# Kernel tuning notes

Measured on AMD Instinct MI355X. Metric: run time of the kernel, lower is better.

Reference implementation:

```python
import jax, jax.numpy as jnp
import numpy as np

EMB = 128
N_LEFT = 100000
N_RIGHT = 100000
N_EDGES = 600000
EDGE_FEAT = 1


def _ortho(key, shape):
    a = jax.random.normal(key, shape, dtype=jnp.float32)
    q, r = jnp.linalg.qr(a if shape[0] >= shape[1] else a.T)
    q = q * jnp.sign(jnp.diag(r))
    return q if shape[0] >= shape[1] else q.T


def setup_inputs() -> dict:
    key = jax.random.key(0)
    ks = jax.random.split(key, 12)
    return {
        "left_features": jax.random.normal(ks[0], (N_LEFT, EMB), dtype=jnp.float32),
        "edge_indices": jax.random.randint(ks[1], (2, N_EDGES), 0, N_LEFT, dtype=jnp.int32).astype(jnp.int64),
        "edge_features": jax.random.normal(ks[2], (N_EDGES, EDGE_FEAT), dtype=jnp.float32),
        "right_features": jax.random.normal(ks[3], (N_RIGHT, EMB), dtype=jnp.float32),
        "scatter_out_size": N_RIGHT,
        # parameters (orthogonal weights, zero biases, unit PreNorm scales)
        "W_left": _ortho(ks[4], (EMB, EMB)),
        "b_left": jnp.zeros((EMB,), jnp.float32),
        "W_edge": _ortho(ks[5], (EMB, EDGE_FEAT)),
        "W_right": _ortho(ks[6], (EMB, EMB)),
        "scale_final": jnp.ones((1,), jnp.float32),
        "W_final": _ortho(ks[7], (EMB, EMB)),
        "b_final": jnp.zeros((EMB,), jnp.float32),
        "scale_post": jnp.ones((1,), jnp.float32),
        "W_out1": _ortho(ks[8], (EMB, 2 * EMB)),
        "b_out1": jnp.zeros((EMB,), jnp.float32),
        "W_out2": _ortho(ks[9], (EMB, EMB)),
        "b_out2": jnp.zeros((EMB,), jnp.float32),
    }


def reference(left_features, edge_indices, edge_features, right_features,
              scatter_out_size, W_left, b_left, W_edge, W_right,
              scale_final, W_final, b_final, scale_post,
              W_out1, b_out1, W_out2, b_out2):
    # node / edge projections
    left_proj = left_features @ W_left.T + b_left            # [n_left, emb]
    edge_proj = edge_features @ W_edge.T                     # [n_edges, emb]
    right_proj = right_features @ W_right.T                  # [n_right, emb]
    # gather per-edge messages and combine
    joint = left_proj[edge_indices[0]] + edge_proj + right_proj[edge_indices[1]]
    # feature_module_final: PreNorm(scale only) -> ReLU -> Linear
    joint = jax.nn.relu(joint * scale_final) @ W_final.T + b_final
    # scatter-add onto right-side nodes (right_to_left=False)
    conv = jax.ops.segment_sum(joint, edge_indices[1], num_segments=scatter_out_size)
    conv = conv * scale_post
    # output MLP on [conv ; prev_right]
    h = jnp.concatenate([conv, right_features], axis=1)      # [n_right, 2*emb]
    h = jax.nn.relu(h @ W_out1.T + b_out1)
    return h @ W_out2.T + b_out2
```

## Files before the change

### kernel.cpp

```cpp
#include <hip/hip_runtime.h>

#define EMB 128

typedef __attribute__((ext_vector_type(8))) short short8;
typedef __attribute__((ext_vector_type(4))) short short4v;
typedef __attribute__((ext_vector_type(4))) float floatx4;

#define MFMA(a, b, c) __builtin_amdgcn_mfma_f32_16x16x32_bf16((a), (b), (c), 0, 0, 0)

__device__ __forceinline__ ushort f2b(float f) {
    unsigned u = __float_as_uint(f);
    return (ushort)((u + 0x7fff + ((u >> 16) & 1)) >> 16);
}
__device__ __forceinline__ float b2f(ushort h) {
    return __uint_as_float(((unsigned)h) << 16);
}
__device__ __forceinline__ short8 cvt8(const float* p) {
    float4 f0 = *(const float4*)p;
    float4 f1 = *(const float4*)(p + 4);
    short8 v;
    v[0] = f2b(f0.x); v[1] = f2b(f0.y); v[2] = f2b(f0.z); v[3] = f2b(f0.w);
    v[4] = f2b(f1.x); v[5] = f2b(f1.y); v[6] = f2b(f1.z); v[7] = f2b(f1.w);
    return v;
}

template <int RSH>
__device__ __forceinline__ void stage32k(const ushort* __restrict__ g,
                                         ushort* __restrict__ lds, int t) {
#pragma unroll
    for (int i = 0; i < 8; i++) {
        int a = i * 4096 + t * 16;
        short8 v = *(const short8*)(g + (a >> 1));
        int d = a ^ (((a >> RSH) & 7) << 4);
        *(short8*)((char*)lds + d) = v;
    }
}
__device__ __forceinline__ short8 ldsW8(const ushort* lds, int byte) {
    return *(const short8*)((const char*)lds + (byte ^ (((byte >> 8) & 7) << 4)));
}
__device__ __forceinline__ short8 ldsW9(const ushort* lds, int byte) {
    return *(const short8*)((const char*)lds + (byte ^ (((byte >> 9) & 7) << 4)));
}

__global__ __launch_bounds__(256) void k_cvthist(const float* __restrict__ w0,
                                                 const float* __restrict__ w1,
                                                 const float* __restrict__ w2,
                                                 const float* __restrict__ w3,
                                                 const float* __restrict__ w4,
                                                 ushort* __restrict__ dst,
                                                 const int* __restrict__ eidx,
                                                 int* __restrict__ cnt,
                                                 int n_edges) {
    int bid = blockIdx.x;
    if (bid < 384) {
        int i = bid * 256 + threadIdx.x;
        const float* src; int off;
        if (i < 16384)      { src = w0; off = i; }
        else if (i < 32768) { src = w1; off = i - 16384; }
        else if (i < 49152) { src = w2; off = i - 32768; }
        else if (i < 81920) { src = w3; off = i - 49152; }
        else                { src = w4; off = i - 81920; }
        dst[i] = f2b(src[off]);
    } else {
        int e = (bid - 384) * 256 + threadIdx.x;
        if (e < n_edges) atomicAdd(&cnt[eidx[n_edges + e]], 1);
    }
}

#define SCAN_CHUNK 4096
__global__ __launch_bounds__(1024) void k_scan1(const int* __restrict__ cnt,
                                                int* __restrict__ offs,
                                                int* __restrict__ bsum, int n) {
    __shared__ int buf[1024];
    int t = threadIdx.x;
    int i0 = blockIdx.x * SCAN_CHUNK + t * 4;
    int v[4];
#pragma unroll
    for (int u = 0; u < 4; u++) { int i = i0 + u; v[u] = (i < n) ? cnt[i] : 0; }
    int s = v[0] + v[1] + v[2] + v[3];
    buf[t] = s;
    __syncthreads();
    for (int d = 1; d < 1024; d <<= 1) {
        int x = (t >= d) ? buf[t - d] : 0;
        __syncthreads();
        buf[t] += x;
        __syncthreads();
    }
    int excl = buf[t] - s;
#pragma unroll
    for (int u = 0; u < 4; u++) { int i = i0 + u; if (i < n) offs[i] = excl; excl += v[u]; }
    if (t == 1023) bsum[blockIdx.x] = buf[1023];
}

__global__ __launch_bounds__(1024) void k_scan2(const int* __restrict__ bsum,
                                                int* __restrict__ offs,
                                                int* __restrict__ cursor, int n) {
    int bid = blockIdx.x;
    int base = 0;
    for (int j = 0; j < bid; j++) base += bsum[j];
    int i0 = bid * SCAN_CHUNK + threadIdx.x * 4;
#pragma unroll
    for (int u = 0; u < 4; u++) {
        int i = i0 + u;
        if (i < n) { int o = offs[i] + base; offs[i] = o; cursor[i] = o; }
    }
}

__global__ __launch_bounds__(256) void k_permproj(const int* __restrict__ eidx,
                                                  const float* __restrict__ ef,
                                                  int* __restrict__ cursor,
                                                  int2* __restrict__ sle,
                                                  int n_edges,
                                                  const float* __restrict__ XL,
                                                  const float* __restrict__ XR,
                                                  const ushort* __restrict__ WLb,
                                                  const ushort* __restrict__ WRb,
                                                  const float* __restrict__ bias,
                                                  ushort* __restrict__ YL,
                                                  ushort* __restrict__ YR,
                                                  int n, int eb, int nblk) {
    __shared__ ushort Wlds[16384];
    int bid = blockIdx.x;
    if (bid < eb) {
        int e = bid * 256 + threadIdx.x;
        if (e < n_edges) {
            int r = eidx[n_edges + e];
            int p = atomicAdd(&cursor[r], 1);
            int2 v; v.x = eidx[e]; v.y = __float_as_int(ef[e]);
            sle[p] = v;
        }
        return;
    }
    bid -= eb;
    const float* X; const ushort* Wb; ushort* Y; int has_bias;
    if (bid < nblk) { X = XL; Wb = WLb; Y = YL; has_bias = 1; }
    else            { X = XR; Wb = WRb; Y = YR; has_bias = 0; bid -= nblk; }

    int t = threadIdx.x, wave = t >> 6, lane = t & 63;
    int m = lane & 15, quad = lane >> 4;
    size_t row0 = (size_t)bid * 64;
    size_t row = row0 + wave * 16 + m;
    size_t rowc = (row < (size_t)n) ? row : (size_t)(n - 1);

    stage32k<8>(Wb, Wlds, t);

    short8 xf[4];
    const float* xr = X + rowc * EMB;
#pragma unroll
    for (int ks = 0; ks < 4; ks++)
        xf[ks] = cvt8(xr + ks * 32 + quad * 8);

    __syncthreads();

    bool ok = (row < (size_t)n);
#pragma unroll
    for (int wt = 0; wt < 8; wt++) {
        floatx4 acc = {0.f, 0.f, 0.f, 0.f};
#pragma unroll
        for (int ks = 0; ks < 4; ks++) {
            short8 w = ldsW8(Wlds, ((wt * 16 + m) << 8) + (ks << 6) + (quad << 4));
            acc = MFMA(w, xf[ks], acc);
        }
        float b0 = 0.f, b1_ = 0.f, b2_ = 0.f, b3 = 0.f;
        if (has_bias) {
            float4 bb = *(const float4*)(bias + wt * 16 + quad * 4);
            b0 = bb.x; b1_ = bb.y; b2_ = bb.z; b3 = bb.w;
        }
        if (ok) {
            short4v o;
            o[0] = f2b(acc[0] + b0);
            o[1] = f2b(acc[1] + b1_);
            o[2] = f2b(acc[2] + b2_);
            o[3] = f2b(acc[3] + b3);
            *(short4v*)(Y + row * EMB + wt * 16 + quad * 4) = o;
        }
    }
}

__global__ __launch_bounds__(256) void k_reduce(const ushort* __restrict__ Pl,
                                                const ushort* __restrict__ Pr,
                                                const int2* __restrict__ sle,
                                                const float* __restrict__ We,
                                                const int* __restrict__ offs,
                                                const float* __restrict__ scale_final,
                                                ushort* __restrict__ S,
                                                int n_right, int n_edges) {
    int r = blockIdx.x * 4 + (threadIdx.x >> 6);
    if (r >= n_right) return;
    int lane = threadIdx.x & 63;
    int g = lane >> 4;
    int m = lane & 15;
    float scale = scale_final[0];

    float4 w0 = *(const float4*)(We + m * 8);
    float4 w1 = *(const float4*)(We + m * 8 + 4);
    short8 prv = *(const short8*)(Pr + (size_t)r * EMB + m * 8);
    float we[8], pr[8];
    we[0] = w0.x; we[1] = w0.y; we[2] = w0.z; we[3] = w0.w;
    we[4] = w1.x; we[5] = w1.y; we[6] = w1.z; we[7] = w1.w;
#pragma unroll
    for (int j = 0; j < 8; j++) pr[j] = b2f((ushort)prv[j]);

    float acc[8] = {0.f, 0.f, 0.f, 0.f, 0.f, 0.f, 0.f, 0.f};
    int s0 = offs[r];
    int s1 = (r + 1 < n_right) ? offs[r + 1] : n_edges;
    int e = s0 + g;
    for (; e + 4 < s1; e += 8) {
        int2 ea = sle[e];
        int2 eb = sle[e + 4];
        short8 pa = *(const short8*)(Pl + (size_t)ea.x * EMB + m * 8);
        short8 pb = *(const short8*)(Pl + (size_t)eb.x * EMB + m * 8);
        float fa = __int_as_float(ea.y), fb = __int_as_float(eb.y);
#pragma unroll
        for (int j = 0; j < 8; j++) {
            acc[j] += fmaxf((b2f((ushort)pa[j]) + pr[j] + fa * we[j]) * scale, 0.f);
            acc[j] += fmaxf((b2f((ushort)pb[j]) + pr[j] + fb * we[j]) * scale, 0.f);
        }
    }
    if (e < s1) {
        int2 ea = sle[e];
        short8 pa = *(const short8*)(Pl + (size_t)ea.x * EMB + m * 8);
        float fa = __int_as_float(ea.y);
#pragma unroll
        for (int j = 0; j < 8; j++)
            acc[j] += fmaxf((b2f((ushort)pa[j]) + pr[j] + fa * we[j]) * scale, 0.f);
    }
#pragma unroll
    for (int j = 0; j < 8; j++) {
        acc[j] += __shfl_xor(acc[j], 16);
        acc[j] += __shfl_xor(acc[j], 32);
    }
    if (g == 0) {
        short8 o;
#pragma unroll
        for (int j = 0; j < 8; j++) o[j] = f2b(acc[j]);
        *(short8*)(S + (size_t)r * EMB + m * 8) = o;
    }
}

__global__ __launch_bounds__(256) void k_out(const ushort* __restrict__ S,
                                             const float* __restrict__ right,
                                             const ushort* __restrict__ Wfb,
                                             const float* __restrict__ bf,
                                             const int* __restrict__ deg,
                                             const float* __restrict__ sc_post,
                                             const ushort* __restrict__ W1b,
                                             const float* __restrict__ b1,
                                             const ushort* __restrict__ W2b,
                                             const float* __restrict__ b2,
                                             float* __restrict__ out, int n) {
    __shared__ ushort Wlds[16384];
    __shared__ ushort H[64][136];
    __shared__ float degs[64];
    int t = threadIdx.x, wave = t >> 6, lane = t & 63;
    int m = lane & 15, quad = lane >> 4;
    size_t row0 = (size_t)blockIdx.x * 64;
    int rl = wave * 16 + m;
    size_t xrow = row0 + rl;
    size_t xrowc = (xrow < (size_t)n) ? xrow : (size_t)(n - 1);
    bool ok = (xrow < (size_t)n);
    float sp = sc_post[0];

    short8 s4[4], ar[4];
    const ushort* sr = S + xrowc * EMB;
    const float* rr = right + xrowc * EMB;
#pragma unroll
    for (int ks = 0; ks < 4; ks++)
        s4[ks] = *(const short8*)(sr + ks * 32 + quad * 8);
    stage32k<8>(Wfb, Wlds, t);
#pragma unroll
    for (int ks = 0; ks < 4; ks++)
        ar[ks] = cvt8(rr + ks * 32 + quad * 8);
    if (t < 64) {
        size_t rr2 = row0 + t;
        degs[t] = (rr2 < (size_t)n) ? (float)deg[rr2] : 0.f;
    }
    __syncthreads();
    float dd = degs[rl];

#pragma unroll
    for (int wt = 0; wt < 8; wt++) {
        floatx4 acc = {0.f, 0.f, 0.f, 0.f};
#pragma unroll
        for (int ks = 0; ks < 4; ks++) {
            short8 w = ldsW8(Wlds, ((wt * 16 + m) << 8) + (ks << 6) + (quad << 4));
            acc = MFMA(w, s4[ks], acc);
        }
        float4 bb = *(const float4*)(bf + wt * 16 + quad * 4);
        short4v o;
        o[0] = f2b((acc[0] + dd * bb.x) * sp);
        o[1] = f2b((acc[1] + dd * bb.y) * sp);
        o[2] = f2b((acc[2] + dd * bb.z) * sp);
        o[3] = f2b((acc[3] + dd * bb.w) * sp);
        *(short4v*)(&H[rl][wt * 16 + quad * 4]) = o;
    }
    short8 c4[4];
#pragma unroll
    for (int ks = 0; ks < 4; ks++)
        c4[ks] = *(const short8*)(&H[rl][ks * 32 + quad * 8]);
    __syncthreads();
    stage32k<9>(W1b, Wlds, t);
    __syncthreads();

#pragma unroll
    for (int wt = 0; wt < 4; wt++) {
        floatx4 acc = {0.f, 0.f, 0.f, 0.f};
        int rb = wt * 16 + m;
#pragma unroll
        for (int ks = 0; ks < 4; ks++) {
            short8 w = ldsW9(Wlds, (rb << 9) + (ks << 6) + (quad << 4));
            acc = MFMA(w, c4[ks], acc);
        }
#pragma unroll
        for (int ks = 0; ks < 4; ks++) {
            short8 w = ldsW9(Wlds, (rb << 9) + 256 + (ks << 6) + (quad << 4));
            acc = MFMA(w, ar[ks], acc);
        }
        float4 bb = *(const float4*)(b1 + wt * 16 + quad * 4);
        short4v o;
        o[0] = f2b(fmaxf(acc[0] + bb.x, 0.f));
        o[1] = f2b(fmaxf(acc[1] + bb.y, 0.f));
        o[2] = f2b(fmaxf(acc[2] + bb.z, 0.f));
        o[3] = f2b(fmaxf(acc[3] + bb.w, 0.f));
        *(short4v*)(&H[rl][wt * 16 + quad * 4]) = o;
    }
    __syncthreads();
    stage32k<9>(W1b + 16384, Wlds, t);
    __syncthreads();

#pragma unroll
    for (int wt = 4; wt < 8; wt++) {
        floatx4 acc = {0.f, 0.f, 0.f, 0.f};
        int rb = (wt - 4) * 16 + m;
#pragma unroll
        for (int ks = 0; ks < 4; ks++) {
            short8 w = ldsW9(Wlds, (rb << 9) + (ks << 6) + (quad << 4));
            acc = MFMA(w, c4[ks], acc);
        }
#pragma unroll
        for (int ks = 0; ks < 4; ks++) {
            short8 w = ldsW9(Wlds, (rb << 9) + 256 + (ks << 6) + (quad << 4));
            acc = MFMA(w, ar[ks], acc);
        }
        float4 bb = *(const float4*)(b1 + wt * 16 + quad * 4);
        short4v o;
        o[0] = f2b(fmaxf(acc[0] + bb.x, 0.f));
        o[1] = f2b(fmaxf(acc[1] + bb.y, 0.f));
        o[2] = f2b(fmaxf(acc[2] + bb.z, 0.f));
        o[3] = f2b(fmaxf(acc[3] + bb.w, 0.f));
        *(short4v*)(&H[rl][wt * 16 + quad * 4]) = o;
    }
    short8 h4[4];
#pragma unroll
    for (int ks = 0; ks < 4; ks++)
        h4[ks] = *(const short8*)(&H[rl][ks * 32 + quad * 8]);
    __syncthreads();
    stage32k<8>(W2b, Wlds, t);
    __syncthreads();

#pragma unroll
    for (int wt = 0; wt < 8; wt++) {
        floatx4 acc = {0.f, 0.f, 0.f, 0.f};
#pragma unroll
        for (int ks = 0; ks < 4; ks++) {
            short8 w = ldsW8(Wlds, ((wt * 16 + m) << 8) + (ks << 6) + (quad << 4));
            acc = MFMA(w, h4[ks], acc);
        }
        if (ok) {
            float4 bb = *(const float4*)(b2 + wt * 16 + quad * 4);
            float4 o;
            o.x = acc[0] + bb.x;
            o.y = acc[1] + bb.y;
            o.z = acc[2] + bb.z;
            o.w = acc[3] + bb.w;
            *(float4*)(out + xrow * EMB + wt * 16 + quad * 4) = o;
        }
    }
}

extern "C" void kernel_launch(void* const* d_in, const int* in_sizes, int n_in,
                              void* d_out, int out_size, void* d_ws, size_t ws_size,
                              hipStream_t stream) {
    const float* left   = (const float*)d_in[0];
    const int*   eidx   = (const int*)  d_in[1];
    const float* efeat  = (const float*)d_in[2];
    const float* right  = (const float*)d_in[3];
    const float* W_left = (const float*)d_in[5];
    const float* b_left = (const float*)d_in[6];
    const float* W_edge = (const float*)d_in[7];
    const float* W_right= (const float*)d_in[8];
    const float* sc_fin = (const float*)d_in[9];
    const float* W_fin  = (const float*)d_in[10];
    const float* b_fin  = (const float*)d_in[11];
    const float* sc_post= (const float*)d_in[12];
    const float* W_out1 = (const float*)d_in[13];
    const float* b_out1 = (const float*)d_in[14];
    const float* W_out2 = (const float*)d_in[15];
    const float* b_out2 = (const float*)d_in[16];

    int n_left  = in_sizes[0] / EMB;
    int n_edges = in_sizes[2];
    int n_right = in_sizes[3] / EMB;

    ushort* us = (ushort*)d_ws;
    ushort* Wl_b = us;
    ushort* Wr_b = us + 16384;
    ushort* Wf_b = us + 32768;
    ushort* W1_b = us + 49152;
    ushort* W2_b = us + 81920;
    ushort* Pl   = us + 98304;
    ushort* Pr   = Pl + (size_t)n_left * EMB;
    ushort* S    = Pr + (size_t)n_right * EMB;
    int* cnt    = (int*)(S + (size_t)n_right * EMB);
    int* offs   = cnt + n_right;
    int* cursor = offs + n_right;
    int* bsum   = cursor + n_right;
    int2* sle   = (int2*)(bsum + 64);

    hipMemsetAsync(cnt, 0, (size_t)n_right * sizeof(int), stream);

    int eb = (n_edges + 255) / 256;
    int nblk = (n_left + 63) / 64;

    k_cvthist<<<384 + eb, 256, 0, stream>>>(W_left, W_right, W_fin, W_out1,
                                            W_out2, us, eidx, cnt, n_edges);

    int nsb = (n_right + SCAN_CHUNK - 1) / SCAN_CHUNK;
    k_scan1<<<nsb, 1024, 0, stream>>>(cnt, offs, bsum, n_right);
    k_scan2<<<nsb, 1024, 0, stream>>>(bsum, offs, cursor, n_right);

    k_permproj<<<eb + 2 * nblk, 256, 0, stream>>>(eidx, efeat, cursor, sle,
                                                  n_edges, left, right,
                                                  Wl_b, Wr_b, b_left,
                                                  Pl, Pr, n_left, eb, nblk);

    k_reduce<<<(n_right + 3) / 4, 256, 0, stream>>>(Pl, Pr, sle, W_edge, offs,
                                                    sc_fin, S, n_right, n_edges);

    k_out<<<(n_right + 63) / 64, 256, 0, stream>>>(S, right, Wf_b, b_fin,
                                                   cnt, sc_post, W1_b, b_out1,
                                                   W2_b, b_out2,
                                                   (float*)d_out, n_right);
}
```

Measured before the change: 350.6 us.

## Make projection blocks persistent with 128-row tiles reusing staged weights

The projection part of k_permproj now launches a fixed 512 blocks per side instead of one block per 64 rows. Each block stages the 32 KB bf16 weight matrix into LDS once and loops over 128-row tiles, with each wave handling two 16-row groups. Each LDS weight fragment feeds two MFMAs. The intent is to amortise weight staging and cut block count, at the cost of fewer blocks to hide memory latency and more registers per thread.

```diff
diff --git a/kernel.cpp b/kernel.cpp
--- a/kernel.cpp
+++ b/kernel.cpp
@@ -106,6 +106,7 @@
     }
 }
 
+#define PROJ_PB 512
 __global__ __launch_bounds__(256) void k_permproj(const int* __restrict__ eidx,
                                                   const float* __restrict__ ef,
                                                   int* __restrict__ cursor,
@@ -118,7 +119,7 @@
                                                   const float* __restrict__ bias,
                                                   ushort* __restrict__ YL,
                                                   ushort* __restrict__ YR,
-                                                  int n, int eb, int nblk) {
+                                                  int n, int eb) {
     __shared__ ushort Wlds[16384];
     int bid = blockIdx.x;
     if (bid < eb) {
@@ -133,46 +134,61 @@
     }
     bid -= eb;
     const float* X; const ushort* Wb; ushort* Y; int has_bias;
-    if (bid < nblk) { X = XL; Wb = WLb; Y = YL; has_bias = 1; }
-    else            { X = XR; Wb = WRb; Y = YR; has_bias = 0; bid -= nblk; }
+    if (bid < PROJ_PB) { X = XL; Wb = WLb; Y = YL; has_bias = 1; }
+    else               { X = XR; Wb = WRb; Y = YR; has_bias = 0; bid -= PROJ_PB; }
 
     int t = threadIdx.x, wave = t >> 6, lane = t & 63;
     int m = lane & 15, quad = lane >> 4;
-    size_t row0 = (size_t)bid * 64;
-    size_t row = row0 + wave * 16 + m;
-    size_t rowc = (row < (size_t)n) ? row : (size_t)(n - 1);
 
     stage32k<8>(Wb, Wlds, t);
-
-    short8 xf[4];
-    const float* xr = X + rowc * EMB;
-#pragma unroll
-    for (int ks = 0; ks < 4; ks++)
-        xf[ks] = cvt8(xr + ks * 32 + quad * 8);
-
-    __syncthreads();
-
-    bool ok = (row < (size_t)n);
-#pragma unroll
-    for (int wt = 0; wt < 8; wt++) {
-        floatx4 acc = {0.f, 0.f, 0.f, 0.f};
-#pragma unroll
-        for (int ks = 0; ks < 4; ks++) {
-            short8 w = ldsW8(Wlds, ((wt * 16 + m) << 8) + (ks << 6) + (quad << 4));
-            acc = MFMA(w, xf[ks], acc);
-        }
-        float b0 = 0.f, b1_ = 0.f, b2_ = 0.f, b3 = 0.f;
-        if (has_bias) {
-            float4 bb = *(const float4*)(bias + wt * 16 + quad * 4);
-            b0 = bb.x; b1_ = bb.y; b2_ = bb.z; b3 = bb.w;
-        }
-        if (ok) {
-            short4v o;
-            o[0] = f2b(acc[0] + b0);
-            o[1] = f2b(acc[1] + b1_);
-            o[2] = f2b(acc[2] + b2_);
-            o[3] = f2b(acc[3] + b3);
-            *(short4v*)(Y + row * EMB + wt * 16 + quad * 4) = o;
+    __syncthreads();
+
+    int ntiles = (n + 127) >> 7;
+    for (int tile = bid; tile < ntiles; tile += PROJ_PB) {
+        size_t base = (size_t)tile * 128 + wave * 32;
+        size_t ra = base + m;
+        size_t rb = base + 16 + m;
+        bool oka = ra < (size_t)n, okb = rb < (size_t)n;
+        size_t rac = oka ? ra : (size_t)(n - 1);
+        size_t rbc = okb ? rb : (size_t)(n - 1);
+        const float* pa = X + rac * EMB;
+        const float* pb = X + rbc * EMB;
+        short8 xa[4], xb[4];
+#pragma unroll
+        for (int ks = 0; ks < 4; ks++) {
+            xa[ks] = cvt8(pa + ks * 32 + quad * 8);
+            xb[ks] = cvt8(pb + ks * 32 + quad * 8);
+        }
+#pragma unroll
+        for (int wt = 0; wt < 8; wt++) {
+            floatx4 a0 = {0.f, 0.f, 0.f, 0.f}, a1 = {0.f, 0.f, 0.f, 0.f};
+#pragma unroll
+            for (int ks = 0; ks < 4; ks++) {
+                short8 w = ldsW8(Wlds, ((wt * 16 + m) << 8) + (ks << 6) + (quad << 4));
+                a0 = MFMA(w, xa[ks], a0);
+                a1 = MFMA(w, xb[ks], a1);
+            }
+            float b0 = 0.f, b1_ = 0.f, b2_ = 0.f, b3 = 0.f;
+            if (has_bias) {
+                float4 bb = *(const float4*)(bias + wt * 16 + quad * 4);
+                b0 = bb.x; b1_ = bb.y; b2_ = bb.z; b3 = bb.w;
+            }
+            if (oka) {
+                short4v o;
+                o[0] = f2b(a0[0] + b0);
+                o[1] = f2b(a0[1] + b1_);
+                o[2] = f2b(a0[2] + b2_);
+                o[3] = f2b(a0[3] + b3);
+                *(short4v*)(Y + ra * EMB + wt * 16 + quad * 4) = o;
+            }
+            if (okb) {
+                short4v o;
+                o[0] = f2b(a1[0] + b0);
+                o[1] = f2b(a1[1] + b1_);
+                o[2] = f2b(a1[2] + b2_);
+                o[3] = f2b(a1[3] + b3);
+                *(short4v*)(Y + rb * EMB + wt * 16 + quad * 4) = o;
+            }
         }
     }
 }
@@ -420,19 +436,18 @@
     hipMemsetAsync(cnt, 0, (size_t)n_right * sizeof(int), stream);
 
     int eb = (n_edges + 255) / 256;
-    int nblk = (n_left + 63) / 64;
+    int nsb = (n_right + SCAN_CHUNK - 1) / SCAN_CHUNK;
 
     k_cvthist<<<384 + eb, 256, 0, stream>>>(W_left, W_right, W_fin, W_out1,
                                             W_out2, us, eidx, cnt, n_edges);
 
-    int nsb = (n_right + SCAN_CHUNK - 1) / SCAN_CHUNK;
     k_scan1<<<nsb, 1024, 0, stream>>>(cnt, offs, bsum, n_right);
     k_scan2<<<nsb, 1024, 0, stream>>>(bsum, offs, cursor, n_right);
 
-    k_permproj<<<eb + 2 * nblk, 256, 0, stream>>>(eidx, efeat, cursor, sle,
-                                                  n_edges, left, right,
-                                                  Wl_b, Wr_b, b_left,
-                                                  Pl, Pr, n_left, eb, nblk);
+    k_permproj<<<eb + 2 * PROJ_PB, 256, 0, stream>>>(eidx, efeat, cursor, sle,
+                                                     n_edges, left, right,
+                                                     Wl_b, Wr_b, b_left,
+                                                     Pl, Pr, n_left, eb);
 
     k_reduce<<<(n_right + 3) / 4, 256, 0, stream>>>(Pl, Pr, sle, W_edge, offs,
                                                     sc_fin, S, n_right, n_edges);
```

Measured after the change: 346.3 us. No clear change (-1.2%).

## Raise rows per block in projection and batch edges per thread in permute

Applied to the files above, without the earlier changes.

The projection part of k_permproj now handles 256 rows per block (64 per wave, four 16-row groups), so each 32KB weight stage to LDS and each LDS weight fragment read is reused across four MFMA row groups instead of one. The edge-permute part now processes four edges per thread with all loads issued before the atomics, which cuts block count and exposes more memory-level parallelism. The trade-offs are higher register pressure from 16 short8 input fragments (launch bounds now ask for 4 blocks), fewer blocks overall, and a coarser tail.

```diff
diff --git a/kernel.cpp b/kernel.cpp
--- a/kernel.cpp
+++ b/kernel.cpp
@@ -106,73 +106,91 @@
     }
 }
 
-__global__ __launch_bounds__(256) void k_permproj(const int* __restrict__ eidx,
-                                                  const float* __restrict__ ef,
-                                                  int* __restrict__ cursor,
-                                                  int2* __restrict__ sle,
-                                                  int n_edges,
-                                                  const float* __restrict__ XL,
-                                                  const float* __restrict__ XR,
-                                                  const ushort* __restrict__ WLb,
-                                                  const ushort* __restrict__ WRb,
-                                                  const float* __restrict__ bias,
-                                                  ushort* __restrict__ YL,
-                                                  ushort* __restrict__ YR,
-                                                  int n, int eb, int nblk) {
+__global__ __launch_bounds__(256, 4) void k_permproj(const int* __restrict__ eidx,
+                                                     const float* __restrict__ ef,
+                                                     int* __restrict__ cursor,
+                                                     int2* __restrict__ sle,
+                                                     int n_edges,
+                                                     const float* __restrict__ XL,
+                                                     const float* __restrict__ XR,
+                                                     const ushort* __restrict__ WLb,
+                                                     const ushort* __restrict__ WRb,
+                                                     const float* __restrict__ bias,
+                                                     ushort* __restrict__ YL,
+                                                     ushort* __restrict__ YR,
+                                                     int n, int ebs, int nblk) {
     __shared__ ushort Wlds[16384];
     int bid = blockIdx.x;
-    if (bid < eb) {
-        int e = bid * 256 + threadIdx.x;
-        if (e < n_edges) {
-            int r = eidx[n_edges + e];
-            int p = atomicAdd(&cursor[r], 1);
-            int2 v; v.x = eidx[e]; v.y = __float_as_int(ef[e]);
-            sle[p] = v;
+    int t = threadIdx.x;
+
+    if (bid < ebs) {
+        int e0 = bid * 1024 + t;
+        int ee[4]; int rr[4]; int ll[4]; float ff[4]; bool vv[4];
+#pragma unroll
+        for (int k = 0; k < 4; k++) {
+            int e = e0 + k * 256;
+            ee[k] = e;
+            vv[k] = e < n_edges;
+            rr[k] = vv[k] ? eidx[n_edges + e] : 0;
+            ll[k] = vv[k] ? eidx[e] : 0;
+            ff[k] = vv[k] ? ef[e] : 0.f;
+        }
+#pragma unroll
+        for (int k = 0; k < 4; k++) {
+            if (vv[k]) {
+                int p = atomicAdd(&cursor[rr[k]], 1);
+                int2 v; v.x = ll[k]; v.y = __float_as_int(ff[k]);
+                sle[p] = v;
+            }
         }
         return;
     }
-    bid -= eb;
+    bid -= ebs;
+
     const float* X; const ushort* Wb; ushort* Y; int has_bias;
     if (bid < nblk) { X = XL; Wb = WLb; Y = YL; has_bias = 1; }
     else            { X = XR; Wb = WRb; Y = YR; has_bias = 0; bid -= nblk; }
 
-    int t = threadIdx.x, wave = t >> 6, lane = t & 63;
+    int wave = t >> 6, lane = t & 63;
     int m = lane & 15, quad = lane >> 4;
-    size_t row0 = (size_t)bid * 64;
-    size_t row = row0 + wave * 16 + m;
-    size_t rowc = (row < (size_t)n) ? row : (size_t)(n - 1);
 
     stage32k<8>(Wb, Wlds, t);
 
-    short8 xf[4];
-    const float* xr = X + rowc * EMB;
-#pragma unroll
-    for (int ks = 0; ks < 4; ks++)
-        xf[ks] = cvt8(xr + ks * 32 + quad * 8);
-
-    __syncthreads();
-
-    bool ok = (row < (size_t)n);
+    size_t base = (size_t)bid * 256 + wave * 64;
+    short8 xf[4][4];
+#pragma unroll
+    for (int g = 0; g < 4; g++) {
+        size_t r = base + g * 16 + m;
+        const float* p = X + ((r < (size_t)n) ? r : (size_t)(n - 1)) * EMB;
+#pragma unroll
+        for (int ks = 0; ks < 4; ks++)
+            xf[g][ks] = cvt8(p + ks * 32 + quad * 8);
+    }
+    __syncthreads();
+
 #pragma unroll
     for (int wt = 0; wt < 8; wt++) {
-        floatx4 acc = {0.f, 0.f, 0.f, 0.f};
-#pragma unroll
-        for (int ks = 0; ks < 4; ks++) {
-            short8 w = ldsW8(Wlds, ((wt * 16 + m) << 8) + (ks << 6) + (quad << 4));
-            acc = MFMA(w, xf[ks], acc);
-        }
-        float b0 = 0.f, b1_ = 0.f, b2_ = 0.f, b3 = 0.f;
-        if (has_bias) {
-            float4 bb = *(const float4*)(bias + wt * 16 + quad * 4);
-            b0 = bb.x; b1_ = bb.y; b2_ = bb.z; b3 = bb.w;
-        }
-        if (ok) {
-            short4v o;
-            o[0] = f2b(acc[0] + b0);
-            o[1] = f2b(acc[1] + b1_);
-            o[2] = f2b(acc[2] + b2_);
-            o[3] = f2b(acc[3] + b3);
-            *(short4v*)(Y + row * EMB + wt * 16 + quad * 4) = o;
+        short8 wv[4];
+#pragma unroll
+        for (int ks = 0; ks < 4; ks++)
+            wv[ks] = ldsW8(Wlds, ((wt * 16 + m) << 8) + (ks << 6) + (quad << 4));
+        float4 bb = {0.f, 0.f, 0.f, 0.f};
+        if (has_bias) bb = *(const float4*)(bias + wt * 16 + quad * 4);
+#pragma unroll
+        for (int g = 0; g < 4; g++) {
+            floatx4 acc = {0.f, 0.f, 0.f, 0.f};
+#pragma unroll
+            for (int ks = 0; ks < 4; ks++)
+                acc = MFMA(wv[ks], xf[g][ks], acc);
+            size_t r = base + g * 16 + m;
+            if (r < (size_t)n) {
+                short4v o;
+                o[0] = f2b(acc[0] + bb.x);
+                o[1] = f2b(acc[1] + bb.y);
+                o[2] = f2b(acc[2] + bb.z);
+                o[3] = f2b(acc[3] + bb.w);
+                *(short4v*)(Y + r * EMB + wt * 16 + quad * 4) = o;
+            }
         }
     }
 }
@@ -419,20 +437,21 @@
 
     hipMemsetAsync(cnt, 0, (size_t)n_right * sizeof(int), stream);
 
-    int eb = (n_edges + 255) / 256;
-    int nblk = (n_left + 63) / 64;
-
-    k_cvthist<<<384 + eb, 256, 0, stream>>>(W_left, W_right, W_fin, W_out1,
-                                            W_out2, us, eidx, cnt, n_edges);
-
+    int ebh = (n_edges + 255) / 256;
+    int ebs = (n_edges + 1023) / 1024;
+    int nblk = (n_left + 255) / 256;
     int nsb = (n_right + SCAN_CHUNK - 1) / SCAN_CHUNK;
+
+    k_cvthist<<<384 + ebh, 256, 0, stream>>>(W_left, W_right, W_fin, W_out1,
+                                             W_out2, us, eidx, cnt, n_edges);
+
     k_scan1<<<nsb, 1024, 0, stream>>>(cnt, offs, bsum, n_right);
     k_scan2<<<nsb, 1024, 0, stream>>>(bsum, offs, cursor, n_right);
 
-    k_permproj<<<eb + 2 * nblk, 256, 0, stream>>>(eidx, efeat, cursor, sle,
-                                                  n_edges, left, right,
-                                                  Wl_b, Wr_b, b_left,
-                                                  Pl, Pr, n_left, eb, nblk);
+    k_permproj<<<ebs + 2 * nblk, 256, 0, stream>>>(eidx, efeat, cursor, sle,
+                                                   n_edges, left, right,
+                                                   Wl_b, Wr_b, b_left,
+                                                   Pl, Pr, n_left, ebs, nblk);
 
     k_reduce<<<(n_right + 3) / 4, 256, 0, stream>>>(Pl, Pr, sle, W_edge, offs,
                                                     sc_fin, S, n_right, n_edges);
```

Result: slower. 377.9 us (+7.8%).

## Make projection kernel persistent with double-buffered async LDS staging of X tiles

Applied to the files above, without the earlier changes.

The projection part of k_permproj becomes persistent: a fixed grid of 384 blocks per side loops over 16-row tiles, instead of one block per 64 rows each restaging the 32KB weight matrix. Each wave keeps its 32-column weight slice and bias in registers across tiles. The next X tile is prefetched into a double-buffered LDS area using global_load_lds with a swizzle, so loads overlap the MFMA work. This cuts repeated weight staging and hides load latency, at the cost of fewer blocks in flight, a barrier per tile, and assuming n_left equals n_right for both sides.

```diff
diff --git a/kernel.cpp b/kernel.cpp
--- a/kernel.cpp
+++ b/kernel.cpp
@@ -40,6 +40,31 @@
 }
 __device__ __forceinline__ short8 ldsW9(const ushort* lds, int byte) {
     return *(const short8*)((const char*)lds + (byte ^ (((byte >> 9) & 7) << 4)));
+}
+
+__device__ __forceinline__ void gld16(const float* gp, void* lbase) {
+    __builtin_amdgcn_global_load_lds(
+        (const __attribute__((address_space(1))) unsigned int*)gp,
+        (__attribute__((address_space(3))) unsigned int*)lbase, 16, 0, 0);
+}
+
+__device__ __forceinline__ void stageX(const float* __restrict__ X, int n,
+                                       float* buf, int tile, int wave, int lane) {
+    size_t R0 = (size_t)tile * 16;
+    const char* base = (const char*)(X + R0 * EMB);
+#pragma unroll
+    for (int i = 0; i < 2; i++) {
+        int abase = i * 4096 + wave * 1024;
+        int a = abase + lane * 16;
+        int src = a ^ (((a >> 9) & 7) << 4);
+        int rl = src >> 9;
+        if (R0 + (size_t)rl >= (size_t)n) rl = (int)((size_t)(n - 1) - R0);
+        const float* gp = (const float*)(base + (size_t)rl * 512 + (src & 511));
+        gld16(gp, (char*)buf + abase);
+    }
+}
+__device__ __forceinline__ float4 ldsX(const float* buf, int byte) {
+    return *(const float4*)((const char*)buf + (byte ^ (((byte >> 9) & 7) << 4)));
 }
 
 __global__ __launch_bounds__(256) void k_cvthist(const float* __restrict__ w0,
@@ -106,6 +131,7 @@
     }
 }
 
+#define PB 384
 __global__ __launch_bounds__(256) void k_permproj(const int* __restrict__ eidx,
                                                   const float* __restrict__ ef,
                                                   int* __restrict__ cursor,
@@ -118,11 +144,14 @@
                                                   const float* __restrict__ bias,
                                                   ushort* __restrict__ YL,
                                                   ushort* __restrict__ YR,
-                                                  int n, int eb, int nblk) {
+                                                  int n, int eb) {
     __shared__ ushort Wlds[16384];
+    __shared__ float Xlds[2][2048];
     int bid = blockIdx.x;
+    int t = threadIdx.x;
+
     if (bid < eb) {
-        int e = bid * 256 + threadIdx.x;
+        int e = bid * 256 + t;
         if (e < n_edges) {
             int r = eidx[n_edges + e];
             int p = atomicAdd(&cursor[r], 1);
@@ -132,48 +161,68 @@
         return;
     }
     bid -= eb;
+
     const float* X; const ushort* Wb; ushort* Y; int has_bias;
-    if (bid < nblk) { X = XL; Wb = WLb; Y = YL; has_bias = 1; }
-    else            { X = XR; Wb = WRb; Y = YR; has_bias = 0; bid -= nblk; }
-
-    int t = threadIdx.x, wave = t >> 6, lane = t & 63;
+    if (bid < PB) { X = XL; Wb = WLb; Y = YL; has_bias = 1; }
+    else          { X = XR; Wb = WRb; Y = YR; has_bias = 0; bid -= PB; }
+
+    int wave = t >> 6, lane = t & 63;
     int m = lane & 15, quad = lane >> 4;
-    size_t row0 = (size_t)bid * 64;
-    size_t row = row0 + wave * 16 + m;
-    size_t rowc = (row < (size_t)n) ? row : (size_t)(n - 1);
+    int colbase = wave * 32;
+    int ntiles = (n + 15) >> 4;
 
     stage32k<8>(Wb, Wlds, t);
-
-    short8 xf[4];
-    const float* xr = X + rowc * EMB;
-#pragma unroll
-    for (int ks = 0; ks < 4; ks++)
-        xf[ks] = cvt8(xr + ks * 32 + quad * 8);
-
-    __syncthreads();
-
-    bool ok = (row < (size_t)n);
-#pragma unroll
-    for (int wt = 0; wt < 8; wt++) {
-        floatx4 acc = {0.f, 0.f, 0.f, 0.f};
-#pragma unroll
-        for (int ks = 0; ks < 4; ks++) {
-            short8 w = ldsW8(Wlds, ((wt * 16 + m) << 8) + (ks << 6) + (quad << 4));
-            acc = MFMA(w, xf[ks], acc);
-        }
-        float b0 = 0.f, b1_ = 0.f, b2_ = 0.f, b3 = 0.f;
-        if (has_bias) {
-            float4 bb = *(const float4*)(bias + wt * 16 + quad * 4);
-            b0 = bb.x; b1_ = bb.y; b2_ = bb.z; b3 = bb.w;
-        }
-        if (ok) {
-            short4v o;
-            o[0] = f2b(acc[0] + b0);
-            o[1] = f2b(acc[1] + b1_);
-            o[2] = f2b(acc[2] + b2_);
-            o[3] = f2b(acc[3] + b3);
-            *(short4v*)(Y + row * EMB + wt * 16 + quad * 4) = o;
-        }
+    stageX(X, n, Xlds[0], bid, wave, lane);
+    __syncthreads();
+
+    short8 wv[2][4];
+    float4 bbv[2];
+#pragma unroll
+    for (int ct = 0; ct < 2; ct++) {
+#pragma unroll
+        for (int ks = 0; ks < 4; ks++)
+            wv[ct][ks] = ldsW8(Wlds, ((colbase + ct * 16 + m) << 8) + (ks << 6) + (quad << 4));
+        if (has_bias) bbv[ct] = *(const float4*)(bias + colbase + ct * 16 + quad * 4);
+        else { bbv[ct].x = 0.f; bbv[ct].y = 0.f; bbv[ct].z = 0.f; bbv[ct].w = 0.f; }
+    }
+
+    int cur = 0;
+    for (int tile = bid; tile < ntiles; tile += PB) {
+        int nxt = tile + PB;
+        if (nxt < ntiles) stageX(X, n, Xlds[cur ^ 1], nxt, wave, lane);
+
+        const float* xb = Xlds[cur];
+        size_t row = (size_t)tile * 16 + m;
+        bool ok = row < (size_t)n;
+
+        short8 xf[4];
+#pragma unroll
+        for (int ks = 0; ks < 4; ks++) {
+            int b0 = m * 512 + ks * 128 + quad * 32;
+            float4 f0 = ldsX(xb, b0);
+            float4 f1 = ldsX(xb, b0 + 16);
+            short8 v;
+            v[0] = f2b(f0.x); v[1] = f2b(f0.y); v[2] = f2b(f0.z); v[3] = f2b(f0.w);
+            v[4] = f2b(f1.x); v[5] = f2b(f1.y); v[6] = f2b(f1.z); v[7] = f2b(f1.w);
+            xf[ks] = v;
+        }
+#pragma unroll
+        for (int ct = 0; ct < 2; ct++) {
+            floatx4 acc = {0.f, 0.f, 0.f, 0.f};
+#pragma unroll
+            for (int ks = 0; ks < 4; ks++)
+                acc = MFMA(wv[ct][ks], xf[ks], acc);
+            if (ok) {
+                short4v o;
+                o[0] = f2b(acc[0] + bbv[ct].x);
+                o[1] = f2b(acc[1] + bbv[ct].y);
+                o[2] = f2b(acc[2] + bbv[ct].z);
+                o[3] = f2b(acc[3] + bbv[ct].w);
+                *(short4v*)(Y + row * EMB + colbase + ct * 16 + quad * 4) = o;
+            }
+        }
+        __syncthreads();
+        cur ^= 1;
     }
 }
 
@@ -420,19 +469,18 @@
     hipMemsetAsync(cnt, 0, (size_t)n_right * sizeof(int), stream);
 
     int eb = (n_edges + 255) / 256;
-    int nblk = (n_left + 63) / 64;
+    int nsb = (n_right + SCAN_CHUNK - 1) / SCAN_CHUNK;
 
     k_cvthist<<<384 + eb, 256, 0, stream>>>(W_left, W_right, W_fin, W_out1,
                                             W_out2, us, eidx, cnt, n_edges);
 
-    int nsb = (n_right + SCAN_CHUNK - 1) / SCAN_CHUNK;
     k_scan1<<<nsb, 1024, 0, stream>>>(cnt, offs, bsum, n_right);
     k_scan2<<<nsb, 1024, 0, stream>>>(bsum, offs, cursor, n_right);
 
-    k_permproj<<<eb + 2 * nblk, 256, 0, stream>>>(eidx, efeat, cursor, sle,
-                                                  n_edges, left, right,
-                                                  Wl_b, Wr_b, b_left,
-                                                  Pl, Pr, n_left, eb, nblk);
+    k_permproj<<<eb + 2 * PB, 256, 0, stream>>>(eidx, efeat, cursor, sle,
+                                                n_edges, left, right,
+                                                Wl_b, Wr_b, b_left,
+                                                Pl, Pr, n_left, eb);
 
     k_reduce<<<(n_right + 3) / 4, 256, 0, stream>>>(Pl, Pr, sle, W_edge, offs,
                                                     sc_fin, S, n_right, n_edges);
```

New measurement: 335.3 us. -4.4%, faster.
